# Performance work log

Measured on AMD Instinct MI355X. Metric: run time of the kernel, lower is better.

Reference implementation:

```python
import jax, jax.numpy as jnp
import numpy as np

B, L, D, N_ITEMS = 512, 100, 128, 100000
ALPHA = 0.3


def setup_inputs() -> dict:
    key = jax.random.key(0)
    ks = jax.random.split(key, 10)
    x = jax.random.randint(ks[0], (B, L), 0, N_ITEMS, dtype=jnp.int32)
    attn_mask = jnp.ones((B, L), dtype=bool)  # unused by forward (parity with torch signature)
    emb = jax.random.normal(ks[1], (N_ITEMS, D), dtype=jnp.float32) * 0.02
    emb = emb.at[0].set(0.0)  # padding_idx=0 row is zeros
    s = 1.0 / np.sqrt(D)
    W_in = jax.random.uniform(ks[2], (D, D), minval=-s, maxval=s, dtype=jnp.float32)
    W_out = jax.random.uniform(ks[3], (D, D), minval=-s, maxval=s, dtype=jnp.float32)
    w_ih = jax.random.uniform(ks[4], (3 * D, D), minval=-s, maxval=s, dtype=jnp.float32)
    w_hh = jax.random.uniform(ks[5], (3 * D, D), minval=-s, maxval=s, dtype=jnp.float32)
    b_ih = jax.random.uniform(ks[6], (3 * D,), minval=-s, maxval=s, dtype=jnp.float32)
    b_hh = jax.random.uniform(ks[7], (3 * D,), minval=-s, maxval=s, dtype=jnp.float32)
    sr = 1.0 / np.sqrt(3 * D)
    W_read = jax.random.uniform(ks[8], (D, 3 * D), minval=-sr, maxval=sr, dtype=jnp.float32)
    b_read = jax.random.uniform(ks[9], (D,), minval=-sr, maxval=sr, dtype=jnp.float32)
    return dict(x=x, attn_mask=attn_mask, emb=emb, W_in=W_in, W_out=W_out,
                w_ih=w_ih, w_hh=w_hh, b_ih=b_ih, b_hh=b_hh, W_read=W_read, b_read=b_read)


def _forward(x, emb, W_in, W_out, w_ih, w_hh, b_ih, b_hh, W_read, b_read):
    n_items, d = emb.shape
    seq_len = x.shape[1]
    BIG = n_items  # sentinel > any item id
    NEG = -1e9

    def per_sample(seq):
        valid = seq != 0
        cnt = valid.sum()
        # --- torch.unique(nonzero, return_inverse=True) via sort + dedup ---
        s = jnp.where(valid, seq, BIG)
        ss = jnp.sort(s)
        prev = jnp.concatenate([jnp.full((1,), -1, ss.dtype), ss[:-1]])
        is_first = (ss != prev) & (ss != BIG)
        n_nodes = is_first.sum()
        rank = jnp.cumsum(is_first) - 1
        nodes_s = jnp.full((seq_len,), BIG, ss.dtype).at[
            jnp.where(is_first, rank, seq_len)].set(ss, mode='drop')  # sorted unique ids, BIG-padded
        node_mask = jnp.arange(seq_len) < n_nodes
        nodes = jnp.where(node_mask, nodes_s, 0)  # pad slots -> item 0 (zero emb row)
        inv = jnp.searchsorted(nodes_s, s)  # inverse indices for valid positions
        # compact nonzero items preserving order (for consecutive-pair edges)
        pos = jnp.cumsum(valid) - 1
        cidx = jnp.where(valid, pos, seq_len)
        compact_inv = jnp.zeros((seq_len,), inv.dtype).at[cidx].set(inv, mode='drop')
        compact_seq = jnp.zeros((seq_len,), seq.dtype).at[cidx].set(seq, mode='drop')
        last_tok = compact_seq[jnp.maximum(cnt - 1, 0)]
        src, dst = compact_inv[:-1], compact_inv[1:]
        edge_mask = jnp.arange(seq_len - 1) < cnt - 1
        # --- message passing: index_add + degree normalize ---
        H0 = emb[nodes]  # [L, d]
        Hin = H0 @ W_in.T
        Hout = H0 @ W_out.T
        dst_safe = jnp.where(edge_mask, dst, seq_len)
        agg = jnp.zeros((seq_len, d), H0.dtype).at[dst_safe].add(
            jnp.where(edge_mask[:, None], Hout[src], 0.0), mode='drop')
        deg = jnp.zeros((seq_len,), H0.dtype).at[dst_safe].add(1.0, mode='drop')
        deg = jnp.maximum(deg, 1.0)
        xin = Hin + agg / deg[:, None]
        # --- GRUCell(xin, H0), torch gate order (r, z, n) ---
        gi = xin @ w_ih.T + b_ih
        gh = H0 @ w_hh.T + b_hh
        gi_r, gi_z, gi_n = jnp.split(gi, 3, axis=-1)
        gh_r, gh_z, gh_n = jnp.split(gh, 3, axis=-1)
        r = jax.nn.sigmoid(gi_r + gh_r)
        z = jax.nn.sigmoid(gi_z + gh_z)
        nct = jnp.tanh(gi_n + r * gh_n)
        H = (1.0 - z) * nct + z * H0
        H = jnp.where(node_mask[:, None], H, 0.0)  # drop padded node slots
        # --- attention readout anchored at last item ---
        li = jnp.clip(jnp.searchsorted(nodes_s, last_tok), 0, seq_len - 1)
        h_last = H[li]
        scores = jnp.where(node_mask, H @ h_last, NEG)
        att = jax.nn.softmax(scores)
        local = att @ H
        gvec = jnp.zeros((d,), H.dtype)  # cooc is None -> zeros_like(local)
        h_read = jnp.tanh(W_read @ jnp.concatenate([h_last, local, ALPHA * gvec]) + b_read)
        row = h_read @ emb.T  # tied output weights
        default = jnp.full((n_items,), NEG, row.dtype).at[0].set(0.0)
        return jnp.where(cnt >= 2, row, default)

    return jax.vmap(per_sample)(x)


def reference(x, attn_mask, emb, W_in, W_out, w_ih, w_hh, b_ih, b_hh, W_read, b_read):
    return _forward(x, emb, W_in, W_out, w_ih, w_hh, b_ih, b_hh, W_read, b_read)
```

## Files before the change

kernel.cpp:

```cpp
#include <hip/hip_runtime.h>
#include <math.h>

#define BATCH 512
#define SEQL  100
#define DIM   128
#define NITEMS 100000
#define NEGV  -1000000000.0f

#define OFF_WINT   98304
#define OFF_WOUTT  114688
#define OFF_WREADT 131072
#define OFF_HREAD  180224
#define OFF_DEG    245760
#define OFF_XIN    296960
#define OFF_HOUT   6850560
#define OFF_NODES_I 13404160
#define OFF_SRC_I   13455360
#define OFF_DST_I   13506048
#define OFF_INFO_I  13556736
#define OFF_WPACK_F 13558784

typedef __attribute__((ext_vector_type(8))) short bf16x8;
typedef __attribute__((ext_vector_type(4))) short s16x4;
typedef __attribute__((ext_vector_type(4))) float f32x4;

__device__ __forceinline__ unsigned short bf16_rne(float x) {
  unsigned int u = __float_as_uint(x);
  unsigned int r = u + 0x7FFFu + ((u >> 16) & 1u);
  return (unsigned short)(r >> 16);
}
__device__ __forceinline__ float bf16_to_f(unsigned short h) {
  return __uint_as_float(((unsigned int)h) << 16);
}

__global__ void k_prep(const float* __restrict__ w_ih, const float* __restrict__ w_hh,
                       const float* __restrict__ W_in, const float* __restrict__ W_out,
                       const float* __restrict__ W_read, float* __restrict__ ws,
                       unsigned short* __restrict__ wpack) {
  int idx = blockIdx.x * 256 + threadIdx.x;
  if (idx < 98304) {
    int mat = idx / 49152, rem = idx % 49152;
    int n = rem / 128, k = rem % 128;
    float v = (mat ? w_hh : w_ih)[rem];
    unsigned short hi = bf16_rne(v);
    unsigned short lo = bf16_rne(v - bf16_to_f(hi));
    int nt = n >> 4, nn = n & 15, c = k >> 5, quad = (k >> 3) & 3, j = k & 7;
    int lane = quad * 16 + nn;
    size_t base = ((size_t)((mat * 24 + nt) * 4 + c)) * 1024 + (size_t)lane * 8 + j;
    wpack[base] = hi;
    wpack[base + 512] = lo;
  }
  if (idx < 49152) {
    int i = idx / 384, jj = idx % 384;
    ws[OFF_WREADT + jj * 128 + i] = W_read[idx];
  }
  if (idx < 16384) {
    int j = idx / 128, k = idx % 128;
    ws[OFF_WINT  + k * 128 + j] = W_in[idx];
    ws[OFF_WOUTT + k * 128 + j] = W_out[idx];
  }
}

__global__ void k_build(const int* __restrict__ x, int* __restrict__ nodes,
                        float* __restrict__ deg, int* __restrict__ esrc,
                        int* __restrict__ edst, int* __restrict__ info) {
  int b = blockIdx.x, tid = threadIdx.x;
  __shared__ int sseq[SEQL];
  __shared__ int sfo[SEQL];
  __shared__ unsigned char sisf[SEQL];
  __shared__ int srank[SEQL];
  __shared__ int spos[SEQL];
  __shared__ int scinv[SEQL];
  __shared__ float sdeg[SEQL];
  __shared__ int s_nn, s_cnt;

  if (tid < SEQL) sseq[tid] = x[b * SEQL + tid];
  __syncthreads();
  int t = (tid < SEQL) ? sseq[tid] : 0;
  bool valid = (tid < SEQL) && (t != 0);
  int f = tid;
  if (valid) {
    for (int j = 0; j < tid; ++j) {
      if (sseq[j] == t) { f = j; break; }
    }
  }
  if (tid < SEQL) {
    sfo[tid] = f;
    sisf[tid] = (valid && f == tid) ? 1 : 0;
    sdeg[tid] = 0.f;
  }
  __syncthreads();
  if (tid == 0) {
    int nn = 0, c = 0;
    for (int i = 0; i < SEQL; ++i) {
      srank[i] = nn; nn += sisf[i];
      spos[i] = c;  c += (sseq[i] != 0) ? 1 : 0;
    }
    s_nn = nn; s_cnt = c;
  }
  __syncthreads();
  int nn = s_nn, cnt = s_cnt;
  if (valid) scinv[spos[tid]] = srank[sfo[tid]];
  __syncthreads();
  if (tid < SEQL) {
    if (sisf[tid]) nodes[b * SEQL + srank[tid]] = t;
    if (tid >= nn) nodes[b * SEQL + tid] = 0;
  }
  __syncthreads();
  if (tid == 0) {
    int ec = (cnt >= 2) ? cnt - 1 : 0;
    for (int e = 0; e < ec; ++e) {
      int s = scinv[e], dnode = scinv[e + 1];
      esrc[b * 99 + e] = s;
      edst[b * 99 + e] = dnode;
      sdeg[dnode] += 1.f;
    }
    info[b * 4 + 0] = ec;
    info[b * 4 + 1] = (cnt >= 1) ? scinv[cnt - 1] : 0;
    info[b * 4 + 2] = (cnt >= 2) ? 1 : 0;
    info[b * 4 + 3] = nn;
  }
  __syncthreads();
  if (tid < SEQL) deg[b * SEQL + tid] = fmaxf(sdeg[tid], 1.f);
}

__global__ __launch_bounds__(256) void k_gemm_inout(
    const float* __restrict__ emb, const float* __restrict__ ws,
    const int* __restrict__ nodes, float* __restrict__ xin, float* __restrict__ hout) {
  __shared__ float Xs[64 * 128];
  int tid = threadIdx.x;
  int rowbase = blockIdx.x * 64;
  const float4* emb4 = (const float4*)emb;
  float4* Xs4 = (float4*)Xs;
  for (int e = tid; e < 64 * 32; e += 256) {
    int r = e >> 5, c4 = e & 31;
    int tok = nodes[rowbase + r];
    Xs4[e] = emb4[(size_t)tok * 32 + c4];
  }
  __syncthreads();
  int jt = tid & 31;
  int rt = tid >> 5;
  const float4* Wi4 = (const float4*)(ws + OFF_WINT);
  const float4* Wo4 = (const float4*)(ws + OFF_WOUTT);
  float accI[8][4]; float accO[8][4];
  #pragma unroll
  for (int r = 0; r < 8; ++r)
    #pragma unroll
    for (int j = 0; j < 4; ++j) { accI[r][j] = 0.f; accO[r][j] = 0.f; }

  for (int k0 = 0; k0 < 128; k0 += 4) {
    float wi[4][4], wo[4][4];
    #pragma unroll
    for (int kk = 0; kk < 4; ++kk) {
      float4 a = Wi4[(k0 + kk) * 32 + jt];
      wi[kk][0] = a.x; wi[kk][1] = a.y; wi[kk][2] = a.z; wi[kk][3] = a.w;
      float4 o = Wo4[(k0 + kk) * 32 + jt];
      wo[kk][0] = o.x; wo[kk][1] = o.y; wo[kk][2] = o.z; wo[kk][3] = o.w;
    }
    #pragma unroll
    for (int r = 0; r < 8; ++r) {
      float4 xv4 = Xs4[(rt * 8 + r) * 32 + (k0 >> 2)];
      float xv[4] = {xv4.x, xv4.y, xv4.z, xv4.w};
      #pragma unroll
      for (int kk = 0; kk < 4; ++kk)
        #pragma unroll
        for (int jj = 0; jj < 4; ++jj) {
          accI[r][jj] = fmaf(xv[kk], wi[kk][jj], accI[r][jj]);
          accO[r][jj] = fmaf(xv[kk], wo[kk][jj], accO[r][jj]);
        }
    }
  }
  float4* xin4 = (float4*)xin;
  float4* hout4 = (float4*)hout;
  #pragma unroll
  for (int r = 0; r < 8; ++r) {
    int row = rowbase + rt * 8 + r;
    float4 vI = {accI[r][0], accI[r][1], accI[r][2], accI[r][3]};
    float4 vO = {accO[r][0], accO[r][1], accO[r][2], accO[r][3]};
    xin4[(size_t)row * 32 + jt] = vI;
    hout4[(size_t)row * 32 + jt] = vO;
  }
}

__global__ void k_scatter(const float* __restrict__ hout, float* __restrict__ xin,
                          const float* __restrict__ deg, const int* __restrict__ esrc,
                          const int* __restrict__ edst, const int* __restrict__ info) {
  int b = blockIdx.x, k = threadIdx.x;
  __shared__ float agg[SEQL * DIM];
  for (int n = 0; n < SEQL; ++n) agg[n * DIM + k] = 0.f;
  int ec = info[b * 4 + 0];
  for (int e = 0; e < ec; ++e) {
    int s = esrc[b * 99 + e], dn = edst[b * 99 + e];
    agg[dn * DIM + k] += hout[((size_t)(b * SEQL + s)) * DIM + k];
  }
  for (int n = 0; n < SEQL; ++n) {
    float dg = deg[b * SEQL + n];
    size_t idx = ((size_t)(b * SEQL + n)) * DIM + k;
    xin[idx] += agg[n * DIM + k] / dg;
  }
}

#define GPAD 136
__global__ __launch_bounds__(128) void k_gru(
    const float* __restrict__ emb, const int* __restrict__ nodes,
    const unsigned short* __restrict__ wpack, const float* __restrict__ xin,
    const float* __restrict__ b_ih, const float* __restrict__ b_hh,
    const int* __restrict__ info, float* __restrict__ Hbuf) {
  __shared__ unsigned short Xhi[32 * GPAD];
  __shared__ unsigned short Xlo[32 * GPAD];
  __shared__ unsigned short Hhi[32 * GPAD];
  __shared__ unsigned short Hlo[32 * GPAD];
  int tid = threadIdx.x;
  int rowbase = blockIdx.x * 32;
  const float4* emb4 = (const float4*)emb;
  const float4* xin4 = (const float4*)xin;
  for (int e = tid; e < 32 * 32; e += 128) {
    int r = e >> 5, c4 = e & 31;
    int row = rowbase + r;
    float4 xv = xin4[(size_t)row * 32 + c4];
    int tok = nodes[row];
    float4 hv = emb4[(size_t)tok * 32 + c4];
    int base = r * GPAD + c4 * 4;
    float xs[4] = {xv.x, xv.y, xv.z, xv.w};
    float hs[4] = {hv.x, hv.y, hv.z, hv.w};
    #pragma unroll
    for (int q = 0; q < 4; ++q) {
      unsigned short xh = bf16_rne(xs[q]);
      Xhi[base + q] = xh; Xlo[base + q] = bf16_rne(xs[q] - bf16_to_f(xh));
      unsigned short hh = bf16_rne(hs[q]);
      Hhi[base + q] = hh; Hlo[base + q] = bf16_rne(hs[q] - bf16_to_f(hh));
    }
  }
  __syncthreads();
  int wave = tid >> 6, lane = tid & 63;
  int quad = lane >> 4, nIdx = lane & 15;
  int mrow = wave * 16 + nIdx;
  bf16x8 aXh[4], aXl[4], aHh[4], aHl[4];
  #pragma unroll
  for (int c = 0; c < 4; ++c) {
    int off = mrow * GPAD + c * 32 + quad * 8;
    aXh[c] = *(const bf16x8*)&Xhi[off];
    aXl[c] = *(const bf16x8*)&Xlo[off];
    aHh[c] = *(const bf16x8*)&Hhi[off];
    aHl[c] = *(const bf16x8*)&Hlo[off];
  }
  int grows[4]; int zm[4];
  #pragma unroll
  for (int i = 0; i < 4; ++i) {
    int grow = rowbase + wave * 16 + quad * 4 + i;
    grows[i] = grow;
    int bs = grow / SEQL;
    int n = grow - bs * SEQL;
    zm[i] = (n < info[bs * 4 + 3]) ? 1 : 0;
  }

  for (int t = 0; t < 8; ++t) {
    f32x4 acc[3][2];
    #pragma unroll
    for (int g = 0; g < 3; ++g)
      #pragma unroll
      for (int m = 0; m < 2; ++m) acc[g][m] = (f32x4){0.f, 0.f, 0.f, 0.f};

    for (int c = 0; c < 4; ++c) {
      bf16x8 Bh[3][2], Bl[3][2];
      #pragma unroll
      for (int g = 0; g < 3; ++g) {
        int nt = g * 8 + t;
        #pragma unroll
        for (int m = 0; m < 2; ++m) {
          size_t bidx = (size_t)((m * 24 + nt) * 4 + c) * 1024 + (size_t)lane * 8;
          Bh[g][m] = *(const bf16x8*)&wpack[bidx];
          Bl[g][m] = *(const bf16x8*)&wpack[bidx + 512];
        }
      }
      #pragma unroll
      for (int g = 0; g < 3; ++g) {
        acc[g][0] = __builtin_amdgcn_mfma_f32_16x16x32_bf16(aXh[c], Bh[g][0], acc[g][0], 0, 0, 0);
        acc[g][1] = __builtin_amdgcn_mfma_f32_16x16x32_bf16(aHh[c], Bh[g][1], acc[g][1], 0, 0, 0);
      }
      #pragma unroll
      for (int g = 0; g < 3; ++g) {
        acc[g][0] = __builtin_amdgcn_mfma_f32_16x16x32_bf16(aXh[c], Bl[g][0], acc[g][0], 0, 0, 0);
        acc[g][1] = __builtin_amdgcn_mfma_f32_16x16x32_bf16(aHh[c], Bl[g][1], acc[g][1], 0, 0, 0);
      }
      #pragma unroll
      for (int g = 0; g < 3; ++g) {
        acc[g][0] = __builtin_amdgcn_mfma_f32_16x16x32_bf16(aXl[c], Bh[g][0], acc[g][0], 0, 0, 0);
        acc[g][1] = __builtin_amdgcn_mfma_f32_16x16x32_bf16(aHl[c], Bh[g][1], acc[g][1], 0, 0, 0);
      }
    }
    int j = t * 16 + nIdx;
    float biR = b_ih[j],       bhR = b_hh[j];
    float biZ = b_ih[128 + j], bhZ = b_hh[128 + j];
    float biN = b_ih[256 + j], bhN = b_hh[256 + j];
    #pragma unroll
    for (int i = 0; i < 4; ++i) {
      float gr = acc[0][0][i] + biR + acc[0][1][i] + bhR;
      float gz = acc[1][0][i] + biZ + acc[1][1][i] + bhZ;
      float r = 1.f / (1.f + expf(-gr));
      float z = 1.f / (1.f + expf(-gz));
      float nct = tanhf(acc[2][0][i] + biN + r * (acc[2][1][i] + bhN));
      int lrow = wave * 16 + quad * 4 + i;
      float h0 = bf16_to_f(Hhi[lrow * GPAD + j]) + bf16_to_f(Hlo[lrow * GPAD + j]);
      float h = (1.f - z) * nct + z * h0;
      if (!zm[i]) h = 0.f;
      Hbuf[(size_t)grows[i] * 128 + j] = h;
    }
  }
}

#define HLS 129
__global__ void k_attn(const float* __restrict__ Hbuf, const float* __restrict__ ws,
                       const float* __restrict__ b_read, const int* __restrict__ info,
                       float* __restrict__ hread) {
  int b = blockIdx.x, tid = threadIdx.x;
  __shared__ float Hl[SEQL * HLS];
  __shared__ float sc[128];
  __shared__ float hl[128];
  __shared__ float att[SEQL];
  __shared__ float loc[128];
  int nn = info[b * 4 + 3], li = info[b * 4 + 1];
  for (int e = tid; e < SEQL * 128; e += 128) {
    int r = e >> 7, k = e & 127;
    Hl[r * HLS + k] = Hbuf[((size_t)(b * SEQL + r)) * DIM + k];
  }
  __syncthreads();
  hl[tid] = Hl[li * HLS + tid];
  __syncthreads();
  float scr = NEGV;
  if (tid < nn) {
    float s = 0.f;
    for (int k = 0; k < 128; ++k) s += Hl[tid * HLS + k] * hl[k];
    scr = s;
  }
  sc[tid] = scr;
  __syncthreads();
  if (tid == 0) {
    float m = sc[0];
    for (int n = 1; n < SEQL; ++n) m = fmaxf(m, sc[n]);
    float sum = 0.f;
    for (int n = 0; n < SEQL; ++n) { float e = expf(sc[n] - m); att[n] = e; sum += e; }
    float inv = 1.f / sum;
    for (int n = 0; n < SEQL; ++n) att[n] *= inv;
  }
  __syncthreads();
  float lv = 0.f;
  for (int n = 0; n < SEQL; ++n) lv = fmaf(att[n], Hl[n * HLS + tid], lv);
  loc[tid] = lv;
  __syncthreads();
  const float* WrT = ws + OFF_WREADT;
  float acc = b_read[tid];
  for (int j = 0; j < 128; ++j) acc = fmaf(WrT[j * 128 + tid], hl[j], acc);
  for (int j = 0; j < 128; ++j) acc = fmaf(WrT[(128 + j) * 128 + tid], loc[j], acc);
  hread[b * 128 + tid] = tanhf(acc);
}

__global__ __launch_bounds__(256) void k_packA(
    const float* __restrict__ hread, unsigned short* __restrict__ apack) {
  int idx = blockIdx.x * 256 + threadIdx.x;
  if (idx >= 8192) return;
  int lane = idx & 63;
  int kc = (idx >> 6) & 3;
  int mt = idx >> 8;
  int quad = lane >> 4, rr = lane & 15;
  int row = mt * 16 + rr;
  int kbase = kc * 32 + quad * 8;
  const float4* hr4 = (const float4*)(hread + row * 128 + kbase);
  float4 v0 = hr4[0], v1 = hr4[1];
  float vs[8] = {v0.x, v0.y, v0.z, v0.w, v1.x, v1.y, v1.z, v1.w};
  bf16x8 hi, lo;
  #pragma unroll
  for (int j = 0; j < 8; ++j) {
    unsigned short h = bf16_rne(vs[j]);
    hi[j] = (short)h;
    lo[j] = (short)bf16_rne(vs[j] - bf16_to_f(h));
  }
  size_t base = ((size_t)(mt * 4 + kc) * 2) * 512 + (size_t)lane * 8;
  *(bf16x8*)&apack[base] = hi;
  *(bf16x8*)&apack[base + 512] = lo;
}

#define EPITCH 136
__global__ __launch_bounds__(256) void k_out(
    const float* __restrict__ emb, const unsigned short* __restrict__ apack,
    const int* __restrict__ info, float* __restrict__ out) {
  __shared__ unsigned short Ehi[64 * EPITCH];
  __shared__ unsigned short Elo[64 * EPITCH];
  int tid = threadIdx.x;
  int b0  = blockIdx.x * 128;
  int it0 = blockIdx.y * 64;

  const float4* emb4 = (const float4*)emb;
  #pragma unroll
  for (int s = 0; s < 8; ++s) {
    int idx = s * 256 + tid;
    int r = idx >> 5, c4 = idx & 31;
    int item = it0 + r;
    float4 v = (item < NITEMS) ? emb4[(size_t)item * 32 + c4]
                               : (float4){0.f, 0.f, 0.f, 0.f};
    float vs[4] = {v.x, v.y, v.z, v.w};
    s16x4 hv, lv;
    #pragma unroll
    for (int q = 0; q < 4; ++q) {
      unsigned short h = bf16_rne(vs[q]);
      hv[q] = (short)h;
      lv[q] = (short)bf16_rne(vs[q] - bf16_to_f(h));
    }
    int base = r * EPITCH + c4 * 4;
    *(s16x4*)&Ehi[base] = hv;
    *(s16x4*)&Elo[base] = lv;
  }
  __syncthreads();

  int wave = tid >> 6, lane = tid & 63;
  int quad = lane >> 4, nIdx = lane & 15;
  int mtg0 = blockIdx.x * 8 + wave * 2;

  bf16x8 ah[2][4], al[2][4];
  #pragma unroll
  for (int m2 = 0; m2 < 2; ++m2)
    #pragma unroll
    for (int kc = 0; kc < 4; ++kc) {
      size_t base = ((size_t)((mtg0 + m2) * 4 + kc) * 2) * 512 + (size_t)lane * 8;
      ah[m2][kc] = *(const bf16x8*)&apack[base];
      al[m2][kc] = *(const bf16x8*)&apack[base + 512];
    }

  f32x4 acc[2][4];
  #pragma unroll
  for (int m2 = 0; m2 < 2; ++m2)
    #pragma unroll
    for (int nt = 0; nt < 4; ++nt) acc[m2][nt] = (f32x4){0.f, 0.f, 0.f, 0.f};

  #pragma unroll
  for (int nt = 0; nt < 4; ++nt) {
    int eoff = (nt * 16 + nIdx) * EPITCH + quad * 8;
    #pragma unroll
    for (int kc = 0; kc < 4; ++kc) {
      bf16x8 Bh = *(const bf16x8*)&Ehi[eoff + kc * 32];
      bf16x8 Bl = *(const bf16x8*)&Elo[eoff + kc * 32];
      acc[0][nt] = __builtin_amdgcn_mfma_f32_16x16x32_bf16(ah[0][kc], Bh, acc[0][nt], 0, 0, 0);
      acc[1][nt] = __builtin_amdgcn_mfma_f32_16x16x32_bf16(ah[1][kc], Bh, acc[1][nt], 0, 0, 0);
      acc[0][nt] = __builtin_amdgcn_mfma_f32_16x16x32_bf16(al[0][kc], Bh, acc[0][nt], 0, 0, 0);
      acc[1][nt] = __builtin_amdgcn_mfma_f32_16x16x32_bf16(al[1][kc], Bh, acc[1][nt], 0, 0, 0);
      acc[0][nt] = __builtin_amdgcn_mfma_f32_16x16x32_bf16(ah[0][kc], Bl, acc[0][nt], 0, 0, 0);
      acc[1][nt] = __builtin_amdgcn_mfma_f32_16x16x32_bf16(ah[1][kc], Bl, acc[1][nt], 0, 0, 0);
    }
  }

  int flags[2][4];
  #pragma unroll
  for (int m2 = 0; m2 < 2; ++m2)
    #pragma unroll
    for (int i = 0; i < 4; ++i) {
      int b = b0 + (wave * 2 + m2) * 16 + quad * 4 + i;
      flags[m2][i] = info[b * 4 + 2];
    }
  #pragma unroll
  for (int m2 = 0; m2 < 2; ++m2)
    #pragma unroll
    for (int nt = 0; nt < 4; ++nt) {
      int item = it0 + nt * 16 + nIdx;
      #pragma unroll
      for (int i = 0; i < 4; ++i) {
        int b = b0 + (wave * 2 + m2) * 16 + quad * 4 + i;
        float v = flags[m2][i] ? acc[m2][nt][i]
                               : ((item == 0) ? 0.f : NEGV);
        if (item < NITEMS) out[(size_t)b * NITEMS + item] = v;
      }
    }
}

extern "C" void kernel_launch(void* const* d_in, const int* in_sizes, int n_in,
                              void* d_out, int out_size, void* d_ws, size_t ws_size,
                              hipStream_t stream) {
  const int*   x      = (const int*)d_in[0];
  const float* emb    = (const float*)d_in[2];
  const float* W_in   = (const float*)d_in[3];
  const float* W_out  = (const float*)d_in[4];
  const float* w_ih   = (const float*)d_in[5];
  const float* w_hh   = (const float*)d_in[6];
  const float* b_ih   = (const float*)d_in[7];
  const float* b_hh   = (const float*)d_in[8];
  const float* W_read = (const float*)d_in[9];
  const float* b_read = (const float*)d_in[10];
  float* ws  = (float*)d_ws;
  int*   wsi = (int*)d_ws;
  unsigned short* wpack = (unsigned short*)(ws + OFF_WPACK_F);
  unsigned short* apack = (unsigned short*)(ws + OFF_XIN);
  float* out = (float*)d_out;

  k_prep<<<384, 256, 0, stream>>>(w_ih, w_hh, W_in, W_out, W_read, ws, wpack);
  k_build<<<BATCH, 128, 0, stream>>>(x, wsi + OFF_NODES_I, ws + OFF_DEG,
                                     wsi + OFF_SRC_I, wsi + OFF_DST_I, wsi + OFF_INFO_I);
  k_gemm_inout<<<800, 256, 0, stream>>>(emb, ws, wsi + OFF_NODES_I,
                                        ws + OFF_XIN, ws + OFF_HOUT);
  k_scatter<<<BATCH, 128, 0, stream>>>(ws + OFF_HOUT, ws + OFF_XIN, ws + OFF_DEG,
                                       wsi + OFF_SRC_I, wsi + OFF_DST_I, wsi + OFF_INFO_I);
  k_gru<<<1600, 128, 0, stream>>>(emb, wsi + OFF_NODES_I, wpack, ws + OFF_XIN,
                                  b_ih, b_hh, wsi + OFF_INFO_I, ws + OFF_HOUT);
  k_attn<<<BATCH, 128, 0, stream>>>(ws + OFF_HOUT, ws, b_read, wsi + OFF_INFO_I,
                                    ws + OFF_HREAD);
  k_packA<<<32, 256, 0, stream>>>(ws + OFF_HREAD, apack);
  k_out<<<dim3(4, 1563), 256, 0, stream>>>(emb, apack, wsi + OFF_INFO_I, out);
}
```

Baseline: 506.5 us.

## Move in/out GEMM to split-bf16 MFMA, prepack embeddings, parallelize softmax, vectorize output

The fp32 FMA in/out projection GEMM becomes a split-bf16 (hi/lo) MFMA kernel that uses prepacked weight fragments. The full embedding table is now packed into MFMA fragment layout once per call by a new k_epack kernel, so k_out no longer converts it per tile and instead reads fragments straight from global memory. k_out's operands are swapped so the accumulator holds four contiguous items per lane, which allows float4 output stores. The serial single-thread softmax in k_attn is replaced by wave shuffle reductions. The cost is an extra pass that reads the table and writes a roughly 51 MB packed copy, which reuses workspace regions such as the old xin area.

```diff
diff --git a/kernel.cpp b/kernel.cpp
--- a/kernel.cpp
+++ b/kernel.cpp
@@ -7,13 +7,12 @@
 #define NITEMS 100000
 #define NEGV  -1000000000.0f
 
-#define OFF_WINT   98304
-#define OFF_WOUTT  114688
 #define OFF_WREADT 131072
 #define OFF_HREAD  180224
 #define OFF_DEG    245760
 #define OFF_XIN    296960
 #define OFF_HOUT   6850560
+#define OFF_EPACK_F (OFF_XIN + 131072)
 #define OFF_NODES_I 13404160
 #define OFF_SRC_I   13455360
 #define OFF_DST_I   13506048
@@ -54,10 +53,18 @@
     int i = idx / 384, jj = idx % 384;
     ws[OFF_WREADT + jj * 128 + i] = W_read[idx];
   }
-  if (idx < 16384) {
-    int j = idx / 128, k = idx % 128;
-    ws[OFF_WINT  + k * 128 + j] = W_in[idx];
-    ws[OFF_WOUTT + k * 128 + j] = W_out[idx];
+  if (idx < 32768) {
+    int mat = idx >> 14, rem = idx & 16383;
+    int n = rem >> 7, k = rem & 127;
+    float v = (mat ? W_out : W_in)[rem];
+    unsigned short hi = bf16_rne(v);
+    unsigned short lo = bf16_rne(v - bf16_to_f(hi));
+    int nt = n >> 4, nn = n & 15, c = k >> 5, quad = (k >> 3) & 3, j = k & 7;
+    int lane = quad * 16 + nn;
+    size_t base = ((size_t)((mat * 8 + nt) * 4 + c)) * 1024 + (size_t)lane * 8 + j;
+    unsigned short* wpack2 = (unsigned short*)ws;
+    wpack2[base] = hi;
+    wpack2[base + 512] = lo;
   }
 }
 
@@ -124,61 +131,64 @@
   if (tid < SEQL) deg[b * SEQL + tid] = fmaxf(sdeg[tid], 1.f);
 }
 
-__global__ __launch_bounds__(256) void k_gemm_inout(
-    const float* __restrict__ emb, const float* __restrict__ ws,
+#define GPAD 136
+__global__ __launch_bounds__(128) void k_gemm_inout(
+    const float* __restrict__ emb, const unsigned short* __restrict__ wpack2,
     const int* __restrict__ nodes, float* __restrict__ xin, float* __restrict__ hout) {
-  __shared__ float Xs[64 * 128];
+  __shared__ unsigned short Hhi[32 * GPAD];
+  __shared__ unsigned short Hlo[32 * GPAD];
   int tid = threadIdx.x;
-  int rowbase = blockIdx.x * 64;
+  int rowbase = blockIdx.x * 32;
   const float4* emb4 = (const float4*)emb;
-  float4* Xs4 = (float4*)Xs;
-  for (int e = tid; e < 64 * 32; e += 256) {
+  for (int e = tid; e < 32 * 32; e += 128) {
     int r = e >> 5, c4 = e & 31;
     int tok = nodes[rowbase + r];
-    Xs4[e] = emb4[(size_t)tok * 32 + c4];
-  }
-  __syncthreads();
-  int jt = tid & 31;
-  int rt = tid >> 5;
-  const float4* Wi4 = (const float4*)(ws + OFF_WINT);
-  const float4* Wo4 = (const float4*)(ws + OFF_WOUTT);
-  float accI[8][4]; float accO[8][4];
-  #pragma unroll
-  for (int r = 0; r < 8; ++r)
-    #pragma unroll
-    for (int j = 0; j < 4; ++j) { accI[r][j] = 0.f; accO[r][j] = 0.f; }
-
-  for (int k0 = 0; k0 < 128; k0 += 4) {
-    float wi[4][4], wo[4][4];
-    #pragma unroll
-    for (int kk = 0; kk < 4; ++kk) {
-      float4 a = Wi4[(k0 + kk) * 32 + jt];
-      wi[kk][0] = a.x; wi[kk][1] = a.y; wi[kk][2] = a.z; wi[kk][3] = a.w;
-      float4 o = Wo4[(k0 + kk) * 32 + jt];
-      wo[kk][0] = o.x; wo[kk][1] = o.y; wo[kk][2] = o.z; wo[kk][3] = o.w;
-    }
-    #pragma unroll
-    for (int r = 0; r < 8; ++r) {
-      float4 xv4 = Xs4[(rt * 8 + r) * 32 + (k0 >> 2)];
-      float xv[4] = {xv4.x, xv4.y, xv4.z, xv4.w};
-      #pragma unroll
-      for (int kk = 0; kk < 4; ++kk)
-        #pragma unroll
-        for (int jj = 0; jj < 4; ++jj) {
-          accI[r][jj] = fmaf(xv[kk], wi[kk][jj], accI[r][jj]);
-          accO[r][jj] = fmaf(xv[kk], wo[kk][jj], accO[r][jj]);
-        }
-    }
-  }
-  float4* xin4 = (float4*)xin;
-  float4* hout4 = (float4*)hout;
-  #pragma unroll
-  for (int r = 0; r < 8; ++r) {
-    int row = rowbase + rt * 8 + r;
-    float4 vI = {accI[r][0], accI[r][1], accI[r][2], accI[r][3]};
-    float4 vO = {accO[r][0], accO[r][1], accO[r][2], accO[r][3]};
-    xin4[(size_t)row * 32 + jt] = vI;
-    hout4[(size_t)row * 32 + jt] = vO;
+    float4 hv = emb4[(size_t)tok * 32 + c4];
+    int base = r * GPAD + c4 * 4;
+    float hs[4] = {hv.x, hv.y, hv.z, hv.w};
+    #pragma unroll
+    for (int q = 0; q < 4; ++q) {
+      unsigned short hh = bf16_rne(hs[q]);
+      Hhi[base + q] = hh;
+      Hlo[base + q] = bf16_rne(hs[q] - bf16_to_f(hh));
+    }
+  }
+  __syncthreads();
+  int wave = tid >> 6, lane = tid & 63;
+  int quad = lane >> 4, nIdx = lane & 15;
+  int mrow = wave * 16 + nIdx;
+  bf16x8 aH[4], aL[4];
+  #pragma unroll
+  for (int c = 0; c < 4; ++c) {
+    int off = mrow * GPAD + c * 32 + quad * 8;
+    aH[c] = *(const bf16x8*)&Hhi[off];
+    aL[c] = *(const bf16x8*)&Hlo[off];
+  }
+  for (int t = 0; t < 8; ++t) {
+    f32x4 accI = (f32x4){0.f, 0.f, 0.f, 0.f};
+    f32x4 accO = (f32x4){0.f, 0.f, 0.f, 0.f};
+    #pragma unroll
+    for (int c = 0; c < 4; ++c) {
+      size_t bi = ((size_t)((0 * 8 + t) * 4 + c)) * 1024 + (size_t)lane * 8;
+      size_t bo = ((size_t)((1 * 8 + t) * 4 + c)) * 1024 + (size_t)lane * 8;
+      bf16x8 BiH = *(const bf16x8*)&wpack2[bi];
+      bf16x8 BiL = *(const bf16x8*)&wpack2[bi + 512];
+      bf16x8 BoH = *(const bf16x8*)&wpack2[bo];
+      bf16x8 BoL = *(const bf16x8*)&wpack2[bo + 512];
+      accI = __builtin_amdgcn_mfma_f32_16x16x32_bf16(aH[c], BiH, accI, 0, 0, 0);
+      accO = __builtin_amdgcn_mfma_f32_16x16x32_bf16(aH[c], BoH, accO, 0, 0, 0);
+      accI = __builtin_amdgcn_mfma_f32_16x16x32_bf16(aL[c], BiH, accI, 0, 0, 0);
+      accO = __builtin_amdgcn_mfma_f32_16x16x32_bf16(aL[c], BoH, accO, 0, 0, 0);
+      accI = __builtin_amdgcn_mfma_f32_16x16x32_bf16(aH[c], BiL, accI, 0, 0, 0);
+      accO = __builtin_amdgcn_mfma_f32_16x16x32_bf16(aH[c], BoL, accO, 0, 0, 0);
+    }
+    int j = t * 16 + nIdx;
+    #pragma unroll
+    for (int i = 0; i < 4; ++i) {
+      size_t row = (size_t)(rowbase + wave * 16 + quad * 4 + i);
+      xin[row * 128 + j]  = accI[i];
+      hout[row * 128 + j] = accO[i];
+    }
   }
 }
 
@@ -200,7 +210,6 @@
   }
 }
 
-#define GPAD 136
 __global__ __launch_bounds__(128) void k_gru(
     const float* __restrict__ emb, const int* __restrict__ nodes,
     const unsigned short* __restrict__ wpack, const float* __restrict__ xin,
@@ -319,6 +328,7 @@
   __shared__ float hl[128];
   __shared__ float att[SEQL];
   __shared__ float loc[128];
+  __shared__ float redm[2], reds[2];
   int nn = info[b * 4 + 3], li = info[b * 4 + 1];
   for (int e = tid; e < SEQL * 128; e += 128) {
     int r = e >> 7, k = e & 127;
@@ -335,14 +345,20 @@
   }
   sc[tid] = scr;
   __syncthreads();
-  if (tid == 0) {
-    float m = sc[0];
-    for (int n = 1; n < SEQL; ++n) m = fmaxf(m, sc[n]);
-    float sum = 0.f;
-    for (int n = 0; n < SEQL; ++n) { float e = expf(sc[n] - m); att[n] = e; sum += e; }
-    float inv = 1.f / sum;
-    for (int n = 0; n < SEQL; ++n) att[n] *= inv;
-  }
+  float m = sc[tid];
+  #pragma unroll
+  for (int o = 32; o >= 1; o >>= 1) m = fmaxf(m, __shfl_xor(m, o, 64));
+  if ((tid & 63) == 0) redm[tid >> 6] = m;
+  __syncthreads();
+  m = fmaxf(redm[0], redm[1]);
+  float e = (tid < SEQL) ? expf(sc[tid] - m) : 0.f;
+  float s = e;
+  #pragma unroll
+  for (int o = 32; o >= 1; o >>= 1) s += __shfl_xor(s, o, 64);
+  if ((tid & 63) == 0) reds[tid >> 6] = s;
+  __syncthreads();
+  float inv = 1.f / (reds[0] + reds[1]);
+  if (tid < SEQL) att[tid] = e * inv;
   __syncthreads();
   float lv = 0.f;
   for (int n = 0; n < SEQL; ++n) lv = fmaf(att[n], Hl[n * HLS + tid], lv);
@@ -380,95 +396,94 @@
   *(bf16x8*)&apack[base + 512] = lo;
 }
 
-#define EPITCH 136
+__global__ __launch_bounds__(256) void k_epack(
+    const float* __restrict__ emb, unsigned short* __restrict__ epack) {
+  int idx = blockIdx.x * 256 + threadIdx.x;
+  int lane = idx & 63;
+  int kc = (idx >> 6) & 3;
+  int it = idx >> 8;
+  int quad = lane >> 4, rr = lane & 15;
+  int row = it * 16 + rr;
+  int kbase = kc * 32 + quad * 8;
+  float4 v0 = {0.f, 0.f, 0.f, 0.f}, v1 = {0.f, 0.f, 0.f, 0.f};
+  if (row < NITEMS) {
+    const float4* p = (const float4*)(emb + (size_t)row * 128 + kbase);
+    v0 = p[0]; v1 = p[1];
+  }
+  float vs[8] = {v0.x, v0.y, v0.z, v0.w, v1.x, v1.y, v1.z, v1.w};
+  bf16x8 hi, lo;
+  #pragma unroll
+  for (int j = 0; j < 8; ++j) {
+    unsigned short h = bf16_rne(vs[j]);
+    hi[j] = (short)h;
+    lo[j] = (short)bf16_rne(vs[j] - bf16_to_f(h));
+  }
+  size_t base = ((size_t)(it * 4 + kc) * 2) * 512 + (size_t)lane * 8;
+  *(bf16x8*)&epack[base] = hi;
+  *(bf16x8*)&epack[base + 512] = lo;
+}
+
 __global__ __launch_bounds__(256) void k_out(
-    const float* __restrict__ emb, const unsigned short* __restrict__ apack,
+    const unsigned short* __restrict__ epack, const unsigned short* __restrict__ apack,
     const int* __restrict__ info, float* __restrict__ out) {
-  __shared__ unsigned short Ehi[64 * EPITCH];
-  __shared__ unsigned short Elo[64 * EPITCH];
   int tid = threadIdx.x;
-  int b0  = blockIdx.x * 128;
-  int it0 = blockIdx.y * 64;
-
-  const float4* emb4 = (const float4*)emb;
-  #pragma unroll
-  for (int s = 0; s < 8; ++s) {
-    int idx = s * 256 + tid;
-    int r = idx >> 5, c4 = idx & 31;
-    int item = it0 + r;
-    float4 v = (item < NITEMS) ? emb4[(size_t)item * 32 + c4]
-                               : (float4){0.f, 0.f, 0.f, 0.f};
-    float vs[4] = {v.x, v.y, v.z, v.w};
-    s16x4 hv, lv;
-    #pragma unroll
-    for (int q = 0; q < 4; ++q) {
-      unsigned short h = bf16_rne(vs[q]);
-      hv[q] = (short)h;
-      lv[q] = (short)bf16_rne(vs[q] - bf16_to_f(h));
-    }
-    int base = r * EPITCH + c4 * 4;
-    *(s16x4*)&Ehi[base] = hv;
-    *(s16x4*)&Elo[base] = lv;
-  }
-  __syncthreads();
-
   int wave = tid >> 6, lane = tid & 63;
   int quad = lane >> 4, nIdx = lane & 15;
-  int mtg0 = blockIdx.x * 8 + wave * 2;
-
-  bf16x8 ah[2][4], al[2][4];
+  int b0   = blockIdx.x * 128;
+  int itt0 = blockIdx.y * 4;
+  int btg0 = blockIdx.x * 8 + wave * 2;
+
+  bf16x8 bh[2][4], bl[2][4];
   #pragma unroll
   for (int m2 = 0; m2 < 2; ++m2)
     #pragma unroll
     for (int kc = 0; kc < 4; ++kc) {
-      size_t base = ((size_t)((mtg0 + m2) * 4 + kc) * 2) * 512 + (size_t)lane * 8;
-      ah[m2][kc] = *(const bf16x8*)&apack[base];
-      al[m2][kc] = *(const bf16x8*)&apack[base + 512];
-    }
-
-  f32x4 acc[2][4];
-  #pragma unroll
-  for (int m2 = 0; m2 < 2; ++m2)
-    #pragma unroll
-    for (int nt = 0; nt < 4; ++nt) acc[m2][nt] = (f32x4){0.f, 0.f, 0.f, 0.f};
-
-  #pragma unroll
-  for (int nt = 0; nt < 4; ++nt) {
-    int eoff = (nt * 16 + nIdx) * EPITCH + quad * 8;
+      size_t base = ((size_t)((btg0 + m2) * 4 + kc) * 2) * 512 + (size_t)lane * 8;
+      bh[m2][kc] = *(const bf16x8*)&apack[base];
+      bl[m2][kc] = *(const bf16x8*)&apack[base + 512];
+    }
+
+  f32x4 acc[4][2];
+  #pragma unroll
+  for (int it = 0; it < 4; ++it)
+    #pragma unroll
+    for (int m2 = 0; m2 < 2; ++m2) acc[it][m2] = (f32x4){0.f, 0.f, 0.f, 0.f};
+
+  #pragma unroll
+  for (int it = 0; it < 4; ++it) {
     #pragma unroll
     for (int kc = 0; kc < 4; ++kc) {
-      bf16x8 Bh = *(const bf16x8*)&Ehi[eoff + kc * 32];
-      bf16x8 Bl = *(const bf16x8*)&Elo[eoff + kc * 32];
-      acc[0][nt] = __builtin_amdgcn_mfma_f32_16x16x32_bf16(ah[0][kc], Bh, acc[0][nt], 0, 0, 0);
-      acc[1][nt] = __builtin_amdgcn_mfma_f32_16x16x32_bf16(ah[1][kc], Bh, acc[1][nt], 0, 0, 0);
-      acc[0][nt] = __builtin_amdgcn_mfma_f32_16x16x32_bf16(al[0][kc], Bh, acc[0][nt], 0, 0, 0);
-      acc[1][nt] = __builtin_amdgcn_mfma_f32_16x16x32_bf16(al[1][kc], Bh, acc[1][nt], 0, 0, 0);
-      acc[0][nt] = __builtin_amdgcn_mfma_f32_16x16x32_bf16(ah[0][kc], Bl, acc[0][nt], 0, 0, 0);
-      acc[1][nt] = __builtin_amdgcn_mfma_f32_16x16x32_bf16(ah[1][kc], Bl, acc[1][nt], 0, 0, 0);
-    }
-  }
-
-  int flags[2][4];
-  #pragma unroll
-  for (int m2 = 0; m2 < 2; ++m2)
-    #pragma unroll
-    for (int i = 0; i < 4; ++i) {
-      int b = b0 + (wave * 2 + m2) * 16 + quad * 4 + i;
-      flags[m2][i] = info[b * 4 + 2];
-    }
-  #pragma unroll
-  for (int m2 = 0; m2 < 2; ++m2)
-    #pragma unroll
-    for (int nt = 0; nt < 4; ++nt) {
-      int item = it0 + nt * 16 + nIdx;
-      #pragma unroll
-      for (int i = 0; i < 4; ++i) {
-        int b = b0 + (wave * 2 + m2) * 16 + quad * 4 + i;
-        float v = flags[m2][i] ? acc[m2][nt][i]
-                               : ((item == 0) ? 0.f : NEGV);
-        if (item < NITEMS) out[(size_t)b * NITEMS + item] = v;
+      size_t abase = ((size_t)((itt0 + it) * 4 + kc) * 2) * 512 + (size_t)lane * 8;
+      bf16x8 Ah = *(const bf16x8*)&epack[abase];
+      bf16x8 Al = *(const bf16x8*)&epack[abase + 512];
+      acc[it][0] = __builtin_amdgcn_mfma_f32_16x16x32_bf16(Ah, bh[0][kc], acc[it][0], 0, 0, 0);
+      acc[it][1] = __builtin_amdgcn_mfma_f32_16x16x32_bf16(Ah, bh[1][kc], acc[it][1], 0, 0, 0);
+      acc[it][0] = __builtin_amdgcn_mfma_f32_16x16x32_bf16(Al, bh[0][kc], acc[it][0], 0, 0, 0);
+      acc[it][1] = __builtin_amdgcn_mfma_f32_16x16x32_bf16(Al, bh[1][kc], acc[it][1], 0, 0, 0);
+      acc[it][0] = __builtin_amdgcn_mfma_f32_16x16x32_bf16(Ah, bl[0][kc], acc[it][0], 0, 0, 0);
+      acc[it][1] = __builtin_amdgcn_mfma_f32_16x16x32_bf16(Ah, bl[1][kc], acc[it][1], 0, 0, 0);
+    }
+  }
+
+  #pragma unroll
+  for (int m2 = 0; m2 < 2; ++m2) {
+    int b = b0 + (wave * 2 + m2) * 16 + nIdx;
+    int flag = info[b * 4 + 2];
+    #pragma unroll
+    for (int it = 0; it < 4; ++it) {
+      int ib = (itt0 + it) * 16 + quad * 4;
+      if (ib < NITEMS) {
+        float4 v;
+        if (flag) {
+          v.x = acc[it][m2][0]; v.y = acc[it][m2][1];
+          v.z = acc[it][m2][2]; v.w = acc[it][m2][3];
+        } else {
+          v.x = (ib == 0) ? 0.f : NEGV; v.y = NEGV; v.z = NEGV; v.w = NEGV;
+        }
+        *(float4*)&out[(size_t)b * NITEMS + ib] = v;
       }
     }
+  }
 }
 
 extern "C" void kernel_launch(void* const* d_in, const int* in_sizes, int n_in,
@@ -486,21 +501,24 @@
   const float* b_read = (const float*)d_in[10];
   float* ws  = (float*)d_ws;
   int*   wsi = (int*)d_ws;
-  unsigned short* wpack = (unsigned short*)(ws + OFF_WPACK_F);
-  unsigned short* apack = (unsigned short*)(ws + OFF_XIN);
+  unsigned short* wpack  = (unsigned short*)(ws + OFF_WPACK_F);
+  unsigned short* wpack2 = (unsigned short*)ws;
+  unsigned short* apack  = (unsigned short*)(ws + OFF_XIN);
+  unsigned short* epack  = (unsigned short*)(ws + OFF_EPACK_F);
   float* out = (float*)d_out;
 
   k_prep<<<384, 256, 0, stream>>>(w_ih, w_hh, W_in, W_out, W_read, ws, wpack);
   k_build<<<BATCH, 128, 0, stream>>>(x, wsi + OFF_NODES_I, ws + OFF_DEG,
                                      wsi + OFF_SRC_I, wsi + OFF_DST_I, wsi + OFF_INFO_I);
-  k_gemm_inout<<<800, 256, 0, stream>>>(emb, ws, wsi + OFF_NODES_I,
-                                        ws + OFF_XIN, ws + OFF_HOUT);
+  k_gemm_inout<<<1600, 128, 0, stream>>>(emb, wpack2, wsi + OFF_NODES_I,
+                                         ws + OFF_XIN, ws + OFF_HOUT);
   k_scatter<<<BATCH, 128, 0, stream>>>(ws + OFF_HOUT, ws + OFF_XIN, ws + OFF_DEG,
                                        wsi + OFF_SRC_I, wsi + OFF_DST_I, wsi + OFF_INFO_I);
   k_gru<<<1600, 128, 0, stream>>>(emb, wsi + OFF_NODES_I, wpack, ws + OFF_XIN,
                                   b_ih, b_hh, wsi + OFF_INFO_I, ws + OFF_HOUT);
   k_attn<<<BATCH, 128, 0, stream>>>(ws + OFF_HOUT, ws, b_read, wsi + OFF_INFO_I,
                                     ws + OFF_HREAD);
+  k_epack<<<6252, 256, 0, stream>>>(emb, epack);
   k_packA<<<32, 256, 0, stream>>>(ws + OFF_HREAD, apack);
-  k_out<<<dim3(4, 1563), 256, 0, stream>>>(emb, apack, wsi + OFF_INFO_I, out);
-}
+  k_out<<<dim3(4, 1563), 256, 0, stream>>>(epack, apack, wsi + OFF_INFO_I, out);
+}
```

Measured after the change: 473.5 us. -6.5%, faster.
